# Optimization experiments

Measured on AMD Instinct MI355X. Metric: run time of the kernel, lower is better.

Reference implementation:

```python
import jax, jax.numpy as jnp
import numpy as np

C = 128
N0, N1, N2 = 1000000, 100000, 10000


def setup_inputs() -> dict:
    key = jax.random.key(0)
    ks = jax.random.split(key, 9)
    return {
        "x0": jax.random.normal(ks[0], (N0, C), dtype=jnp.float32),
        "x1": jax.random.normal(ks[1], (N1, C), dtype=jnp.float32),
        "x2": jax.random.normal(ks[2], (N2, C), dtype=jnp.float32),
        "cluster1": jax.random.randint(ks[3], (N0,), 0, N1, dtype=jnp.int32),
        "cluster2": jax.random.randint(ks[4], (N1,), 0, N2, dtype=jnp.int32),
        "Wf2c0": jax.random.normal(ks[5], (C, C), dtype=jnp.float32) / np.sqrt(C),
        "Wf2c1": jax.random.normal(ks[6], (C, C), dtype=jnp.float32) / np.sqrt(C),
        "Wc2f0": jax.random.normal(ks[7], (C, C), dtype=jnp.float32) / np.sqrt(C),
        "Wc2f1": jax.random.normal(ks[8], (C, C), dtype=jnp.float32) / np.sqrt(C),
    }


def _segment_mean(x, idx, num_segments):
    # scatter-mean: sum per cluster / count (count clamped to 1 -> empty clusters give 0)
    s = jax.ops.segment_sum(x, idx, num_segments=num_segments)
    cnt = jax.ops.segment_sum(jnp.ones((x.shape[0], 1), x.dtype), idx, num_segments=num_segments)
    return s / jnp.maximum(cnt, 1.0)


def reference(x0, x1, x2, cluster1, cluster2, Wf2c0, Wf2c1, Wc2f0, Wc2f1):
    n1, n2 = x1.shape[0], x2.shape[0]
    # scale 0: x0 + gather(coarse_to_fine_0(x1), cluster1)
    y0 = x0 + (x1 @ Wc2f0.T)[cluster1]
    # scale 1: x1 + fine_to_coarse_0(scatter_mean(x0, cluster1)) + gather(coarse_to_fine_1(x2), cluster2)
    y1 = x1 + _segment_mean(x0, cluster1, n1) @ Wf2c0.T + (x2 @ Wc2f1.T)[cluster2]
    # scale 2: x2 + fine_to_coarse_1(scatter_mean(x1, cluster2))
    y2 = x2 + _segment_mean(x1, cluster2, n2) @ Wf2c1.T
    return (y0, y1, y2)
```

## Files before the change

kernel.cpp:

```cpp
#include <hip/hip_runtime.h>

#define C128 128

typedef __attribute__((ext_vector_type(2))) float f32x2;
typedef __attribute__((ext_vector_type(4))) float f32x4;
typedef __attribute__((ext_vector_type(8))) short short8;

__device__ __forceinline__ short f2bf(float f) {
  union { float f; unsigned u; } v; v.f = f;
  unsigned r = (v.u + 0x7fffu + ((v.u >> 16) & 1u)) >> 16;
  return (short)r;
}

__global__ __launch_bounds__(256) void prep(
    const float* __restrict__ Wa, const float* __restrict__ Wb_,
    const float* __restrict__ Wc, const float* __restrict__ Wd,
    ushort* __restrict__ Wout, int* __restrict__ zbuf, int zlen)
{
  const int tid = blockIdx.x * 256 + threadIdx.x;
  const int nth = gridDim.x * 256;
  for (int k = tid; k < zlen; k += nth) zbuf[k] = 0;
  for (int k = tid; k < 4 * 16384; k += nth) {
    const float* W = (k < 16384) ? Wa : (k < 32768) ? Wb_ : (k < 49152) ? Wc : Wd;
    Wout[k] = (ushort)f2bf(W[k & 16383]);
  }
}

__device__ __forceinline__ void gemm_body(
    const float* __restrict__ A, const ushort* __restrict__ Wb,
    const float* __restrict__ add,
    const int* __restrict__ gidx, const float* __restrict__ gtab,
    float* __restrict__ out, int R, int blockrow)
{
  const int tid  = threadIdx.x;
  const int wave = tid >> 6;
  const int lane = tid & 63;
  const int r16  = lane & 15;
  const int kg   = lane >> 4;

  const int rowbase = blockrow + wave * 16;
  if (rowbase >= R) return;
  const int arow_i  = rowbase + r16;
  const int lrow    = arow_i < R ? arow_i : (R - 1);

  f32x4 acc[8];
#pragma unroll
  for (int i = 0; i < 8; ++i) acc[i] = (f32x4){0.f, 0.f, 0.f, 0.f};

  const float* arow = A + (long long)lrow * C128;

#pragma unroll
  for (int ks = 0; ks < 4; ++ks) {
    const int k0 = ks * 32 + kg * 8;
    f32x4 alo = *(const f32x4*)(arow + k0);
    f32x4 ahi = *(const f32x4*)(arow + k0 + 4);
    short8 af;
    af[0] = f2bf(alo.x); af[1] = f2bf(alo.y);
    af[2] = f2bf(alo.z); af[3] = f2bf(alo.w);
    af[4] = f2bf(ahi.x); af[5] = f2bf(ahi.y);
    af[6] = f2bf(ahi.z); af[7] = f2bf(ahi.w);
#pragma unroll
    for (int nf = 0; nf < 8; ++nf) {
      short8 bf = *(const short8*)(Wb + (nf * 16 + r16) * C128 + k0);
      acc[nf] = __builtin_amdgcn_mfma_f32_16x16x32_bf16(af, bf, acc[nf], 0, 0, 0);
    }
  }

#pragma unroll
  for (int i = 0; i < 4; ++i) {
    const int orow = rowbase + kg * 4 + i;
    if (orow >= R) continue;
    const float* addrow = add ? add + (long long)orow * C128 : nullptr;
    const float* grow = gidx ? gtab + (long long)gidx[orow] * C128 : nullptr;
    float* orow_p = out + (long long)orow * C128;
#pragma unroll
    for (int nf = 0; nf < 8; ++nf) {
      const int oc = nf * 16 + r16;
      float v = acc[nf][i];
      if (addrow) v += addrow[oc];
      if (grow)   v += grow[oc];
      orow_p[oc] = v;
    }
  }
}

__global__ __launch_bounds__(256) void pre_hist_gemm(
    const float* __restrict__ x1, const ushort* __restrict__ W1b, float* __restrict__ t1, int n1,
    const float* __restrict__ x2, const ushort* __restrict__ W2b, float* __restrict__ t2, int n2,
    const int* __restrict__ cl1, int n0, int* __restrict__ cnt0,
    const int* __restrict__ cl2, int* __restrict__ cnt1, int B1)
{
  {
    int i = blockIdx.x * 256 + threadIdx.x;
    const int nth = gridDim.x * 256;
    const int total = n0 + n1;
    for (; i < total; i += nth) {
      if (i < n0) atomicAdd(&cnt0[cl1[i]], 1);
      else        atomicAdd(&cnt1[cl2[i - n0]], 1);
    }
  }
  if ((int)blockIdx.x < B1)
    gemm_body(x1, W1b, nullptr, nullptr, nullptr, t1, n1, blockIdx.x * 64);
  else
    gemm_body(x2, W2b, nullptr, nullptr, nullptr, t2, n2, (blockIdx.x - B1) * 64);
}

__global__ __launch_bounds__(256) void post_gemm(
    const float* __restrict__ mean0, const ushort* __restrict__ Wab,
    const float* __restrict__ x1, const int* __restrict__ cluster2,
    const float* __restrict__ t2, float* __restrict__ y1, int n1,
    const float* __restrict__ mean1, const ushort* __restrict__ Wbb,
    const float* __restrict__ x2, float* __restrict__ y2, int n2, int B1)
{
  if ((int)blockIdx.x < B1)
    gemm_body(mean0, Wab, x1, cluster2, t2, y1, n1, blockIdx.x * 64);
  else
    gemm_body(mean1, Wbb, x2, nullptr, nullptr, y2, n2, (blockIdx.x - B1) * 64);
}

__global__ __launch_bounds__(256) void scan2(
    const int* __restrict__ cnt0, int* __restrict__ off0, int* __restrict__ cur0, int n1,
    const int* __restrict__ cnt1, int* __restrict__ off1, int* __restrict__ cur1, int n2,
    int* __restrict__ tot)
{
  const int p1 = (n1 + 255) & ~255;
  const int i  = blockIdx.x * blockDim.x + threadIdx.x;
  const int lane = threadIdx.x & 63;

  const int* cnt; int* off; int* cur; int* t; int j; int nn;
  if (i < p1) { cnt = cnt0; off = off0; cur = cur0; t = tot + 0; j = i;      nn = n1; }
  else        { cnt = cnt1; off = off1; cur = cur1; t = tot + 1; j = i - p1; nn = n2; }

  int c = (j < nn) ? cnt[j] : 0;
  int pref = c;
#pragma unroll
  for (int d = 1; d < 64; d <<= 1) {
    int v = __shfl_up(pref, d);
    if (lane >= d) pref += v;
  }
  const int wave_total = __shfl(pref, 63);
  int base = 0;
  if (lane == 63) base = atomicAdd(t, wave_total);
  base = __shfl(base, 63);

  if (j < nn) {
    const int o = base + (pref - c);
    off[j] = o;
    cur[j] = o;
  }
}

__global__ __launch_bounds__(256) void fill2(
    const int* __restrict__ cl1, int n0, int* __restrict__ cur0, int* __restrict__ idx0,
    const int* __restrict__ cl2, int n1, int* __restrict__ cur1, int* __restrict__ idx1)
{
  int i = blockIdx.x * blockDim.x + threadIdx.x;
  const int stride = gridDim.x * blockDim.x;
  const int total = n0 + n1;
  for (; i < total; i += stride) {
    if (i < n0) { int p = atomicAdd(&cur0[cl1[i]], 1); idx0[p] = i; }
    else        { int k = i - n0; int p = atomicAdd(&cur1[cl2[k]], 1); idx1[p] = k; }
  }
}

__device__ __forceinline__ void cr_one(
    int wid, int lane, const float* __restrict__ x,
    const int* __restrict__ idxp, const int* __restrict__ offp,
    const int* __restrict__ cntp, const float* __restrict__ trow,
    float* __restrict__ yb, float* __restrict__ meanp)
{
  const int n = cntp[wid];
  const int o = offp[wid];

  f32x2 tc = {0.f, 0.f};
  if (trow) tc = ((const f32x2*)trow)[lane];

  f32x2 s0 = {0.f,0.f}, s1 = {0.f,0.f}, s2 = {0.f,0.f}, s3 = {0.f,0.f};
  for (int base = 0; base < n; base += 64) {
    int m = n - base; if (m > 64) m = 64;
    int vi = (lane < m) ? idxp[o + base + lane] : 0;
    int j = 0;
    for (; j + 3 < m; j += 4) {
      const long long i0 = __shfl(vi, j);
      const long long i1 = __shfl(vi, j + 1);
      const long long i2 = __shfl(vi, j + 2);
      const long long i3 = __shfl(vi, j + 3);
      f32x2 a = ((const f32x2*)(x + i0 * C128))[lane];
      f32x2 b = ((const f32x2*)(x + i1 * C128))[lane];
      f32x2 c = ((const f32x2*)(x + i2 * C128))[lane];
      f32x2 d = ((const f32x2*)(x + i3 * C128))[lane];
      s0 += a; s1 += b; s2 += c; s3 += d;
      if (yb) {
        ((f32x2*)(yb + i0 * C128))[lane] = a + tc;
        ((f32x2*)(yb + i1 * C128))[lane] = b + tc;
        ((f32x2*)(yb + i2 * C128))[lane] = c + tc;
        ((f32x2*)(yb + i3 * C128))[lane] = d + tc;
      }
    }
    for (; j < m; ++j) {
      const long long i0 = __shfl(vi, j);
      f32x2 a = ((const f32x2*)(x + i0 * C128))[lane];
      s0 += a;
      if (yb) ((f32x2*)(yb + i0 * C128))[lane] = a + tc;
    }
  }

  const float invn = n > 0 ? 1.0f / (float)n : 0.0f;
  ((f32x2*)(meanp + (long long)wid * C128))[lane] = ((s0 + s1) + (s2 + s3)) * invn;
}

__global__ __launch_bounds__(256) void cluster_reduce2(
    const float* __restrict__ x0, const int* __restrict__ idx0,
    const int* __restrict__ off0, const int* __restrict__ cnt0,
    const float* __restrict__ t1, float* __restrict__ y0,
    float* __restrict__ mean0, int n1,
    const float* __restrict__ x1, const int* __restrict__ idx1,
    const int* __restrict__ off1, const int* __restrict__ cnt1,
    float* __restrict__ mean1, int n2)
{
  const int wid  = blockIdx.x * 4 + (threadIdx.x >> 6);
  const int lane = threadIdx.x & 63;
  if (wid >= n1 + n2) return;

  if (wid < n1)
    cr_one(wid, lane, x0, idx0, off0, cnt0,
           t1 + (long long)wid * C128, y0, mean0);
  else
    cr_one(wid - n1, lane, x1, idx1, off1, cnt1,
           nullptr, nullptr, mean1);
}

extern "C" void kernel_launch(void* const* d_in, const int* in_sizes, int n_in,
                              void* d_out, int out_size, void* d_ws, size_t ws_size,
                              hipStream_t stream)
{
  const float* x0 = (const float*)d_in[0];
  const float* x1 = (const float*)d_in[1];
  const float* x2 = (const float*)d_in[2];
  const int* cluster1 = (const int*)d_in[3];
  const int* cluster2 = (const int*)d_in[4];
  const float* Wf2c0 = (const float*)d_in[5];
  const float* Wf2c1 = (const float*)d_in[6];
  const float* Wc2f0 = (const float*)d_in[7];
  const float* Wc2f1 = (const float*)d_in[8];

  const int N0 = in_sizes[0] / C128;
  const int N1 = in_sizes[1] / C128;
  const int N2 = in_sizes[2] / C128;

  float* y0 = (float*)d_out;
  float* y1 = y0 + (long long)N0 * C128;
  float* y2 = y1 + (long long)N1 * C128;

  float* mean0 = y1;
  float* mean1 = y2;

  float* t1 = (float*)d_ws;
  float* t2 = t1 + (long long)N1 * C128;
  int* cnt0 = (int*)(t2 + (long long)N2 * C128);
  int* cnt1 = cnt0 + N1;
  int* tot  = cnt1 + N2;
  int* off0 = tot + 2;
  int* off1 = off0 + N1;
  int* cur0 = off1 + N2;
  int* cur1 = cur0 + N1;
  int* idx0 = cur1 + N2;
  int* idx1 = idx0 + N0;
  ushort* Wb = (ushort*)(idx1 + N1);
  ushort* Wb_c2f0 = Wb;
  ushort* Wb_c2f1 = Wb + 16384;
  ushort* Wb_f2c0 = Wb + 32768;
  ushort* Wb_f2c1 = Wb + 49152;

  const int B1 = (N1 + 63) / 64;
  const int B2 = (N2 + 63) / 64;

  prep<<<256, 256, 0, stream>>>(
      Wc2f0, Wc2f1, Wf2c0, Wf2c1, Wb, cnt0, N1 + N2 + 2);

  pre_hist_gemm<<<B1 + B2, 256, 0, stream>>>(
      x1, Wb_c2f0, t1, N1, x2, Wb_c2f1, t2, N2,
      cluster1, N0, cnt0, cluster2, cnt1, B1);

  const int p1 = (N1 + 255) & ~255, p2 = (N2 + 255) & ~255;
  scan2<<<(p1 + p2) / 256, 256, 0, stream>>>(
      cnt0, off0, cur0, N1, cnt1, off1, cur1, N2, tot);
  int bh = (N0 + N1 + 255) / 256; if (bh > 2048) bh = 2048;
  fill2<<<bh, 256, 0, stream>>>(cluster1, N0, cur0, idx0, cluster2, N1, cur1, idx1);

  cluster_reduce2<<<(N1 + N2 + 3) / 4, 256, 0, stream>>>(
      x0, idx0, off0, cnt0, t1, y0, mean0, N1,
      x1, idx1, off1, cnt1, mean1, N2);

  post_gemm<<<B1 + B2, 256, 0, stream>>>(
      mean0, Wb_f2c0, x1, cluster2, t2, y1, N1,
      mean1, Wb_f2c1, x2, y2, N2, B1);
}
```

Measured before the change: 499.3 us.

## Stream x0 sequentially into bf16 cluster bins instead of gathering by index

Replaces the fill-index plus gathered cluster reduce with a streaming pass. It reads x0/x1 rows in order, writes y0, and scatters bf16 copies of each row into per-cluster bins using atomic cursors. A second kernel then reduces the contiguous bins into bf16 means, which feed the post GEMM directly as bf16 A operands. The goal is to swap random full-precision gathers of x0 for sequential reads and half-size scattered writes. The cost is extra workspace, a bf16 rounding of the inputs before summation, and a fallback path when the workspace is too small.

```diff
diff --git a/kernel.cpp b/kernel.cpp
--- a/kernel.cpp
+++ b/kernel.cpp
@@ -10,6 +10,12 @@
   union { float f; unsigned u; } v; v.f = f;
   unsigned r = (v.u + 0x7fffu + ((v.u >> 16) & 1u)) >> 16;
   return (short)r;
+}
+
+__device__ __forceinline__ f32x2 bfp2f(unsigned u) {
+  union { unsigned u; float f; } a, b;
+  a.u = u << 16; b.u = u & 0xffff0000u;
+  return (f32x2){a.f, b.f};
 }
 
 __global__ __launch_bounds__(256) void prep(
@@ -26,8 +32,9 @@
   }
 }
 
+template <typename AT>
 __device__ __forceinline__ void gemm_body(
-    const float* __restrict__ A, const ushort* __restrict__ Wb,
+    const AT* __restrict__ A, const ushort* __restrict__ Wb,
     const float* __restrict__ add,
     const int* __restrict__ gidx, const float* __restrict__ gtab,
     float* __restrict__ out, int R, int blockrow)
@@ -47,18 +54,22 @@
 #pragma unroll
   for (int i = 0; i < 8; ++i) acc[i] = (f32x4){0.f, 0.f, 0.f, 0.f};
 
-  const float* arow = A + (long long)lrow * C128;
+  const AT* arow = A + (long long)lrow * C128;
 
 #pragma unroll
   for (int ks = 0; ks < 4; ++ks) {
     const int k0 = ks * 32 + kg * 8;
-    f32x4 alo = *(const f32x4*)(arow + k0);
-    f32x4 ahi = *(const f32x4*)(arow + k0 + 4);
     short8 af;
-    af[0] = f2bf(alo.x); af[1] = f2bf(alo.y);
-    af[2] = f2bf(alo.z); af[3] = f2bf(alo.w);
-    af[4] = f2bf(ahi.x); af[5] = f2bf(ahi.y);
-    af[6] = f2bf(ahi.z); af[7] = f2bf(ahi.w);
+    if constexpr (sizeof(AT) == 2) {
+      af = *(const short8*)((const ushort*)arow + k0);
+    } else {
+      f32x4 alo = *(const f32x4*)((const float*)arow + k0);
+      f32x4 ahi = *(const f32x4*)((const float*)arow + k0 + 4);
+      af[0] = f2bf(alo.x); af[1] = f2bf(alo.y);
+      af[2] = f2bf(alo.z); af[3] = f2bf(alo.w);
+      af[4] = f2bf(ahi.x); af[5] = f2bf(ahi.y);
+      af[6] = f2bf(ahi.z); af[7] = f2bf(ahi.w);
+    }
 #pragma unroll
     for (int nf = 0; nf < 8; ++nf) {
       short8 bf = *(const short8*)(Wb + (nf * 16 + r16) * C128 + k0);
@@ -100,22 +111,9 @@
     }
   }
   if ((int)blockIdx.x < B1)
-    gemm_body(x1, W1b, nullptr, nullptr, nullptr, t1, n1, blockIdx.x * 64);
+    gemm_body<float>(x1, W1b, nullptr, nullptr, nullptr, t1, n1, blockIdx.x * 64);
   else
-    gemm_body(x2, W2b, nullptr, nullptr, nullptr, t2, n2, (blockIdx.x - B1) * 64);
-}
-
-__global__ __launch_bounds__(256) void post_gemm(
-    const float* __restrict__ mean0, const ushort* __restrict__ Wab,
-    const float* __restrict__ x1, const int* __restrict__ cluster2,
-    const float* __restrict__ t2, float* __restrict__ y1, int n1,
-    const float* __restrict__ mean1, const ushort* __restrict__ Wbb,
-    const float* __restrict__ x2, float* __restrict__ y2, int n2, int B1)
-{
-  if ((int)blockIdx.x < B1)
-    gemm_body(mean0, Wab, x1, cluster2, t2, y1, n1, blockIdx.x * 64);
-  else
-    gemm_body(mean1, Wbb, x2, nullptr, nullptr, y2, n2, (blockIdx.x - B1) * 64);
+    gemm_body<float>(x2, W2b, nullptr, nullptr, nullptr, t2, n2, (blockIdx.x - B1) * 64);
 }
 
 __global__ __launch_bounds__(256) void scan2(
@@ -149,6 +147,92 @@
     cur[j] = o;
   }
 }
+
+
+__global__ __launch_bounds__(256) void stream_bin(
+    const float* __restrict__ x0, const int* __restrict__ cl1,
+    const float* __restrict__ t1, float* __restrict__ y0,
+    int* __restrict__ cur0, ushort* __restrict__ bin0, int n0,
+    const float* __restrict__ x1, const int* __restrict__ cl2,
+    int* __restrict__ cur1, ushort* __restrict__ bin1, int n1)
+{
+  const int wid0 = blockIdx.x * 4 + (threadIdx.x >> 6);
+  const int nw   = gridDim.x * 4;
+  const int lane = threadIdx.x & 63;
+  const int total = n0 + n1;
+  for (int r = wid0; r < total; r += nw) {
+    if (r < n0) {
+      const int c = cl1[r];
+      int pos = 0;
+      if (lane == 0) pos = atomicAdd(&cur0[c], 1);
+      pos = __shfl(pos, 0);
+      f32x2 xv = ((const f32x2*)(x0 + (long long)r * C128))[lane];
+      f32x2 tv = ((const f32x2*)(t1 + (long long)c * C128))[lane];
+      ((f32x2*)(y0 + (long long)r * C128))[lane] = xv + tv;
+      unsigned p = ((unsigned)(ushort)f2bf(xv.x)) | (((unsigned)(ushort)f2bf(xv.y)) << 16);
+      ((unsigned*)bin0)[(long long)pos * 64 + lane] = p;
+    } else {
+      const int rr = r - n0;
+      const int c = cl2[rr];
+      int pos = 0;
+      if (lane == 0) pos = atomicAdd(&cur1[c], 1);
+      pos = __shfl(pos, 0);
+      f32x2 xv = ((const f32x2*)(x1 + (long long)rr * C128))[lane];
+      unsigned p = ((unsigned)(ushort)f2bf(xv.x)) | (((unsigned)(ushort)f2bf(xv.y)) << 16);
+      ((unsigned*)bin1)[(long long)pos * 64 + lane] = p;
+    }
+  }
+}
+
+__global__ __launch_bounds__(256) void reduce_bins(
+    const ushort* __restrict__ bin0, const int* __restrict__ off0,
+    const int* __restrict__ cnt0, ushort* __restrict__ mb0, int n1,
+    const ushort* __restrict__ bin1, const int* __restrict__ off1,
+    const int* __restrict__ cnt1, ushort* __restrict__ mb1, int n2)
+{
+  int wid = blockIdx.x * 4 + (threadIdx.x >> 6);
+  const int lane = threadIdx.x & 63;
+  if (wid >= n1 + n2) return;
+
+  const ushort* bin; const int* off; const int* cnt; ushort* mb;
+  if (wid < n1) { bin = bin0; off = off0; cnt = cnt0; mb = mb0; }
+  else { wid -= n1; bin = bin1; off = off1; cnt = cnt1; mb = mb1; }
+
+  const int n = cnt[wid];
+  const long long o = off[wid];
+
+  f32x2 s0 = {0.f,0.f}, s1 = {0.f,0.f}, s2 = {0.f,0.f}, s3 = {0.f,0.f};
+  int m = 0;
+  for (; m + 3 < n; m += 4) {
+    unsigned a = ((const unsigned*)bin)[(o + m) * 64 + lane];
+    unsigned b = ((const unsigned*)bin)[(o + m + 1) * 64 + lane];
+    unsigned c = ((const unsigned*)bin)[(o + m + 2) * 64 + lane];
+    unsigned d = ((const unsigned*)bin)[(o + m + 3) * 64 + lane];
+    s0 += bfp2f(a); s1 += bfp2f(b); s2 += bfp2f(c); s3 += bfp2f(d);
+  }
+  for (; m < n; ++m)
+    s0 += bfp2f(((const unsigned*)bin)[(o + m) * 64 + lane]);
+
+  f32x2 s = (s0 + s1) + (s2 + s3);
+  const float invn = n > 0 ? 1.0f / (float)n : 0.0f;
+  s *= invn;
+  unsigned p = ((unsigned)(ushort)f2bf(s.x)) | (((unsigned)(ushort)f2bf(s.y)) << 16);
+  ((unsigned*)mb)[(long long)wid * 64 + lane] = p;
+}
+
+__global__ __launch_bounds__(256) void post_gemm_b(
+    const ushort* __restrict__ mb0, const ushort* __restrict__ Wab,
+    const float* __restrict__ x1, const int* __restrict__ cluster2,
+    const float* __restrict__ t2, float* __restrict__ y1, int n1,
+    const ushort* __restrict__ mb1, const ushort* __restrict__ Wbb,
+    const float* __restrict__ x2, float* __restrict__ y2, int n2, int B1)
+{
+  if ((int)blockIdx.x < B1)
+    gemm_body<ushort>(mb0, Wab, x1, cluster2, t2, y1, n1, blockIdx.x * 64);
+  else
+    gemm_body<ushort>(mb1, Wbb, x2, nullptr, nullptr, y2, n2, (blockIdx.x - B1) * 64);
+}
+
 
 __global__ __launch_bounds__(256) void fill2(
     const int* __restrict__ cl1, int n0, int* __restrict__ cur0, int* __restrict__ idx0,
@@ -230,6 +314,19 @@
            nullptr, nullptr, mean1);
 }
 
+__global__ __launch_bounds__(256) void post_gemm_f(
+    const float* __restrict__ mean0, const ushort* __restrict__ Wab,
+    const float* __restrict__ x1, const int* __restrict__ cluster2,
+    const float* __restrict__ t2, float* __restrict__ y1, int n1,
+    const float* __restrict__ mean1, const ushort* __restrict__ Wbb,
+    const float* __restrict__ x2, float* __restrict__ y2, int n2, int B1)
+{
+  if ((int)blockIdx.x < B1)
+    gemm_body<float>(mean0, Wab, x1, cluster2, t2, y1, n1, blockIdx.x * 64);
+  else
+    gemm_body<float>(mean1, Wbb, x2, nullptr, nullptr, y2, n2, (blockIdx.x - B1) * 64);
+}
+
 extern "C" void kernel_launch(void* const* d_in, const int* in_sizes, int n_in,
                               void* d_out, int out_size, void* d_ws, size_t ws_size,
                               hipStream_t stream)
@@ -252,31 +349,44 @@
   float* y1 = y0 + (long long)N0 * C128;
   float* y2 = y1 + (long long)N1 * C128;
 
-  float* mean0 = y1;
-  float* mean1 = y2;
-
-  float* t1 = (float*)d_ws;
-  float* t2 = t1 + (long long)N1 * C128;
-  int* cnt0 = (int*)(t2 + (long long)N2 * C128);
-  int* cnt1 = cnt0 + N1;
-  int* tot  = cnt1 + N2;
-  int* off0 = tot + 2;
-  int* off1 = off0 + N1;
-  int* cur0 = off1 + N2;
-  int* cur1 = cur0 + N1;
-  int* idx0 = cur1 + N2;
-  int* idx1 = idx0 + N0;
-  ushort* Wb = (ushort*)(idx1 + N1);
-  ushort* Wb_c2f0 = Wb;
-  ushort* Wb_c2f1 = Wb + 16384;
-  ushort* Wb_f2c0 = Wb + 32768;
-  ushort* Wb_f2c1 = Wb + 49152;
+  float* wsf = (float*)d_ws;
+  long long o = 0;
+  float* t1 = wsf + o;          o += (long long)N1 * C128;
+  float* t2 = wsf + o;          o += (long long)N2 * C128;
+  int* cnt0 = (int*)(wsf + o);  o += N1;
+  int* cnt1 = (int*)(wsf + o);  o += N2;
+  int* tot  = (int*)(wsf + o);  o += 2;
+  int* off0 = (int*)(wsf + o);  o += N1;
+  int* off1 = (int*)(wsf + o);  o += N2;
+  int* cur0 = (int*)(wsf + o);  o += N1;
+  int* cur1 = (int*)(wsf + o);  o += N2;
+  const long long head = o;
+
+  long long oa = (head + 7) & ~7LL;
+  ushort* Wb  = (ushort*)(wsf + oa); oa += 4 * 16384 / 2;
+  ushort* mb0 = (ushort*)(wsf + oa); oa += (long long)N1 * 64;
+  ushort* mb1 = (ushort*)(wsf + oa); oa += (long long)N2 * 64;
+  ushort* bin0 = (ushort*)(wsf + oa); oa += (long long)N0 * 64;
+  ushort* bin1 = (ushort*)(wsf + oa); oa += (long long)N1 * 64;
+  const size_t needA = (size_t)oa * 4;
+
+  long long ob = head;
+  int* idx0 = (int*)(wsf + ob); ob += N0;
+  int* idx1 = (int*)(wsf + ob); ob += N1;
+  ob = (ob + 7) & ~7LL;
+  ushort* WbB = (ushort*)(wsf + ob); ob += 4 * 16384 / 2;
 
   const int B1 = (N1 + 63) / 64;
   const int B2 = (N2 + 63) / 64;
+  const bool bigws = ws_size >= needA;
+  ushort* Wp = bigws ? Wb : WbB;
+  ushort* Wb_c2f0 = Wp;
+  ushort* Wb_c2f1 = Wp + 16384;
+  ushort* Wb_f2c0 = Wp + 32768;
+  ushort* Wb_f2c1 = Wp + 49152;
 
   prep<<<256, 256, 0, stream>>>(
-      Wc2f0, Wc2f1, Wf2c0, Wf2c1, Wb, cnt0, N1 + N2 + 2);
+      Wc2f0, Wc2f1, Wf2c0, Wf2c1, Wp, cnt0, N1 + N2 + 2);
 
   pre_hist_gemm<<<B1 + B2, 256, 0, stream>>>(
       x1, Wb_c2f0, t1, N1, x2, Wb_c2f1, t2, N2,
@@ -285,14 +395,27 @@
   const int p1 = (N1 + 255) & ~255, p2 = (N2 + 255) & ~255;
   scan2<<<(p1 + p2) / 256, 256, 0, stream>>>(
       cnt0, off0, cur0, N1, cnt1, off1, cur1, N2, tot);
-  int bh = (N0 + N1 + 255) / 256; if (bh > 2048) bh = 2048;
-  fill2<<<bh, 256, 0, stream>>>(cluster1, N0, cur0, idx0, cluster2, N1, cur1, idx1);
-
-  cluster_reduce2<<<(N1 + N2 + 3) / 4, 256, 0, stream>>>(
-      x0, idx0, off0, cnt0, t1, y0, mean0, N1,
-      x1, idx1, off1, cnt1, mean1, N2);
-
-  post_gemm<<<B1 + B2, 256, 0, stream>>>(
-      mean0, Wb_f2c0, x1, cluster2, t2, y1, N1,
-      mean1, Wb_f2c1, x2, y2, N2, B1);
-}
+
+  if (bigws) {
+    stream_bin<<<2048, 256, 0, stream>>>(
+        x0, cluster1, t1, y0, cur0, bin0, N0,
+        x1, cluster2, cur1, bin1, N1);
+    reduce_bins<<<(N1 + N2 + 3) / 4, 256, 0, stream>>>(
+        bin0, off0, cnt0, mb0, N1,
+        bin1, off1, cnt1, mb1, N2);
+    post_gemm_b<<<B1 + B2, 256, 0, stream>>>(
+        mb0, Wb_f2c0, x1, cluster2, t2, y1, N1,
+        mb1, Wb_f2c1, x2, y2, N2, B1);
+  } else {
+    float* mean0 = y1;
+    float* mean1 = y2;
+    int bh = (N0 + N1 + 255) / 256; if (bh > 2048) bh = 2048;
+    fill2<<<bh, 256, 0, stream>>>(cluster1, N0, cur0, idx0, cluster2, N1, cur1, idx1);
+    cluster_reduce2<<<(N1 + N2 + 3) / 4, 256, 0, stream>>>(
+        x0, idx0, off0, cnt0, t1, y0, mean0, N1,
+        x1, idx1, off1, cnt1, mean1, N2);
+    post_gemm_f<<<B1 + B2, 256, 0, stream>>>(
+        mean0, Wb_f2c0, x1, cluster2, t2, y1, N1,
+        mean1, Wb_f2c1, x2, y2, N2, B1);
+  }
+}
```

New measurement: 677.2 us. 1.36x slower.

## Regroup launches: fuse histogram with weight conversion, fill with pre-GEMM

Applied to the files above, without the earlier changes.

Moves the cluster histogram into the weight-conversion kernel (zeroing is now a memset) and merges the index-fill pass into the pre-GEMM kernel, so the fill's atomics overlap with the x1/x2 projection GEMMs instead of running as a separate launch. This removes one kernel launch and one serialized pass. It also adds an 8-way unrolled gather loop in the cluster reduce to keep more loads in flight, and aligns the bf16 weight buffer in the workspace. The fill now runs on B1+B2 blocks rather than a capped grid, and the extra unroll raises register pressure.

```diff
diff --git a/kernel.cpp b/kernel.cpp
--- a/kernel.cpp
+++ b/kernel.cpp
@@ -12,17 +12,55 @@
   return (short)r;
 }
 
-__global__ __launch_bounds__(256) void prep(
+__global__ __launch_bounds__(256) void hist_wconv(
+    const int* __restrict__ cl1, int n0, int* __restrict__ cnt0,
+    const int* __restrict__ cl2, int n1, int* __restrict__ cnt1,
     const float* __restrict__ Wa, const float* __restrict__ Wb_,
     const float* __restrict__ Wc, const float* __restrict__ Wd,
-    ushort* __restrict__ Wout, int* __restrict__ zbuf, int zlen)
+    ushort* __restrict__ Wout)
 {
   const int tid = blockIdx.x * 256 + threadIdx.x;
   const int nth = gridDim.x * 256;
-  for (int k = tid; k < zlen; k += nth) zbuf[k] = 0;
   for (int k = tid; k < 4 * 16384; k += nth) {
     const float* W = (k < 16384) ? Wa : (k < 32768) ? Wb_ : (k < 49152) ? Wc : Wd;
     Wout[k] = (ushort)f2bf(W[k & 16383]);
+  }
+  const int total = n0 + n1;
+  for (int i = tid; i < total; i += nth) {
+    if (i < n0) atomicAdd(&cnt0[cl1[i]], 1);
+    else        atomicAdd(&cnt1[cl2[i - n0]], 1);
+  }
+}
+
+__global__ __launch_bounds__(256) void scan2(
+    const int* __restrict__ cnt0, int* __restrict__ off0, int* __restrict__ cur0, int n1,
+    const int* __restrict__ cnt1, int* __restrict__ off1, int* __restrict__ cur1, int n2,
+    int* __restrict__ tot)
+{
+  const int p1 = (n1 + 255) & ~255;
+  const int i  = blockIdx.x * blockDim.x + threadIdx.x;
+  const int lane = threadIdx.x & 63;
+
+  const int* cnt; int* off; int* cur; int* t; int j; int nn;
+  if (i < p1) { cnt = cnt0; off = off0; cur = cur0; t = tot + 0; j = i;      nn = n1; }
+  else        { cnt = cnt1; off = off1; cur = cur1; t = tot + 1; j = i - p1; nn = n2; }
+
+  int c = (j < nn) ? cnt[j] : 0;
+  int pref = c;
+#pragma unroll
+  for (int d = 1; d < 64; d <<= 1) {
+    int v = __shfl_up(pref, d);
+    if (lane >= d) pref += v;
+  }
+  const int wave_total = __shfl(pref, 63);
+  int base = 0;
+  if (lane == 63) base = atomicAdd(t, wave_total);
+  base = __shfl(base, 63);
+
+  if (j < nn) {
+    const int o = base + (pref - c);
+    off[j] = o;
+    cur[j] = o;
   }
 }
 
@@ -84,83 +122,26 @@
   }
 }
 
-__global__ __launch_bounds__(256) void pre_hist_gemm(
-    const float* __restrict__ x1, const ushort* __restrict__ W1b, float* __restrict__ t1, int n1,
-    const float* __restrict__ x2, const ushort* __restrict__ W2b, float* __restrict__ t2, int n2,
-    const int* __restrict__ cl1, int n0, int* __restrict__ cnt0,
-    const int* __restrict__ cl2, int* __restrict__ cnt1, int B1)
+__global__ __launch_bounds__(256) void fill_pregemm(
+    const int* __restrict__ cl1, int n0, int* __restrict__ cur0, int* __restrict__ idx0,
+    const int* __restrict__ cl2, int n1, int* __restrict__ cur1, int* __restrict__ idx1,
+    const float* __restrict__ x1, const ushort* __restrict__ W1b, float* __restrict__ t1,
+    const float* __restrict__ x2, const ushort* __restrict__ W2b, float* __restrict__ t2,
+    int n2, int B1)
 {
   {
     int i = blockIdx.x * 256 + threadIdx.x;
     const int nth = gridDim.x * 256;
     const int total = n0 + n1;
     for (; i < total; i += nth) {
-      if (i < n0) atomicAdd(&cnt0[cl1[i]], 1);
-      else        atomicAdd(&cnt1[cl2[i - n0]], 1);
+      if (i < n0) { int p = atomicAdd(&cur0[cl1[i]], 1); idx0[p] = i; }
+      else        { int k = i - n0; int p = atomicAdd(&cur1[cl2[k]], 1); idx1[p] = k; }
     }
   }
   if ((int)blockIdx.x < B1)
     gemm_body(x1, W1b, nullptr, nullptr, nullptr, t1, n1, blockIdx.x * 64);
   else
     gemm_body(x2, W2b, nullptr, nullptr, nullptr, t2, n2, (blockIdx.x - B1) * 64);
-}
-
-__global__ __launch_bounds__(256) void post_gemm(
-    const float* __restrict__ mean0, const ushort* __restrict__ Wab,
-    const float* __restrict__ x1, const int* __restrict__ cluster2,
-    const float* __restrict__ t2, float* __restrict__ y1, int n1,
-    const float* __restrict__ mean1, const ushort* __restrict__ Wbb,
-    const float* __restrict__ x2, float* __restrict__ y2, int n2, int B1)
-{
-  if ((int)blockIdx.x < B1)
-    gemm_body(mean0, Wab, x1, cluster2, t2, y1, n1, blockIdx.x * 64);
-  else
-    gemm_body(mean1, Wbb, x2, nullptr, nullptr, y2, n2, (blockIdx.x - B1) * 64);
-}
-
-__global__ __launch_bounds__(256) void scan2(
-    const int* __restrict__ cnt0, int* __restrict__ off0, int* __restrict__ cur0, int n1,
-    const int* __restrict__ cnt1, int* __restrict__ off1, int* __restrict__ cur1, int n2,
-    int* __restrict__ tot)
-{
-  const int p1 = (n1 + 255) & ~255;
-  const int i  = blockIdx.x * blockDim.x + threadIdx.x;
-  const int lane = threadIdx.x & 63;
-
-  const int* cnt; int* off; int* cur; int* t; int j; int nn;
-  if (i < p1) { cnt = cnt0; off = off0; cur = cur0; t = tot + 0; j = i;      nn = n1; }
-  else        { cnt = cnt1; off = off1; cur = cur1; t = tot + 1; j = i - p1; nn = n2; }
-
-  int c = (j < nn) ? cnt[j] : 0;
-  int pref = c;
-#pragma unroll
-  for (int d = 1; d < 64; d <<= 1) {
-    int v = __shfl_up(pref, d);
-    if (lane >= d) pref += v;
-  }
-  const int wave_total = __shfl(pref, 63);
-  int base = 0;
-  if (lane == 63) base = atomicAdd(t, wave_total);
-  base = __shfl(base, 63);
-
-  if (j < nn) {
-    const int o = base + (pref - c);
-    off[j] = o;
-    cur[j] = o;
-  }
-}
-
-__global__ __launch_bounds__(256) void fill2(
-    const int* __restrict__ cl1, int n0, int* __restrict__ cur0, int* __restrict__ idx0,
-    const int* __restrict__ cl2, int n1, int* __restrict__ cur1, int* __restrict__ idx1)
-{
-  int i = blockIdx.x * blockDim.x + threadIdx.x;
-  const int stride = gridDim.x * blockDim.x;
-  const int total = n0 + n1;
-  for (; i < total; i += stride) {
-    if (i < n0) { int p = atomicAdd(&cur0[cl1[i]], 1); idx0[p] = i; }
-    else        { int k = i - n0; int p = atomicAdd(&cur1[cl2[k]], 1); idx1[p] = k; }
-  }
 }
 
 __device__ __forceinline__ void cr_one(
@@ -180,6 +161,36 @@
     int m = n - base; if (m > 64) m = 64;
     int vi = (lane < m) ? idxp[o + base + lane] : 0;
     int j = 0;
+    for (; j + 7 < m; j += 8) {
+      const long long i0 = __shfl(vi, j);
+      const long long i1 = __shfl(vi, j + 1);
+      const long long i2 = __shfl(vi, j + 2);
+      const long long i3 = __shfl(vi, j + 3);
+      const long long i4 = __shfl(vi, j + 4);
+      const long long i5 = __shfl(vi, j + 5);
+      const long long i6 = __shfl(vi, j + 6);
+      const long long i7 = __shfl(vi, j + 7);
+      f32x2 a = ((const f32x2*)(x + i0 * C128))[lane];
+      f32x2 b = ((const f32x2*)(x + i1 * C128))[lane];
+      f32x2 c = ((const f32x2*)(x + i2 * C128))[lane];
+      f32x2 d = ((const f32x2*)(x + i3 * C128))[lane];
+      f32x2 e = ((const f32x2*)(x + i4 * C128))[lane];
+      f32x2 f = ((const f32x2*)(x + i5 * C128))[lane];
+      f32x2 g = ((const f32x2*)(x + i6 * C128))[lane];
+      f32x2 h = ((const f32x2*)(x + i7 * C128))[lane];
+      s0 += a; s1 += b; s2 += c; s3 += d;
+      s0 += e; s1 += f; s2 += g; s3 += h;
+      if (yb) {
+        ((f32x2*)(yb + i0 * C128))[lane] = a + tc;
+        ((f32x2*)(yb + i1 * C128))[lane] = b + tc;
+        ((f32x2*)(yb + i2 * C128))[lane] = c + tc;
+        ((f32x2*)(yb + i3 * C128))[lane] = d + tc;
+        ((f32x2*)(yb + i4 * C128))[lane] = e + tc;
+        ((f32x2*)(yb + i5 * C128))[lane] = f + tc;
+        ((f32x2*)(yb + i6 * C128))[lane] = g + tc;
+        ((f32x2*)(yb + i7 * C128))[lane] = h + tc;
+      }
+    }
     for (; j + 3 < m; j += 4) {
       const long long i0 = __shfl(vi, j);
       const long long i1 = __shfl(vi, j + 1);
@@ -230,6 +241,19 @@
            nullptr, nullptr, mean1);
 }
 
+__global__ __launch_bounds__(256) void post_gemm(
+    const float* __restrict__ mean0, const ushort* __restrict__ Wab,
+    const float* __restrict__ x1, const int* __restrict__ cluster2,
+    const float* __restrict__ t2, float* __restrict__ y1, int n1,
+    const float* __restrict__ mean1, const ushort* __restrict__ Wbb,
+    const float* __restrict__ x2, float* __restrict__ y2, int n2, int B1)
+{
+  if ((int)blockIdx.x < B1)
+    gemm_body(mean0, Wab, x1, cluster2, t2, y1, n1, blockIdx.x * 64);
+  else
+    gemm_body(mean1, Wbb, x2, nullptr, nullptr, y2, n2, (blockIdx.x - B1) * 64);
+}
+
 extern "C" void kernel_launch(void* const* d_in, const int* in_sizes, int n_in,
                               void* d_out, int out_size, void* d_ws, size_t ws_size,
                               hipStream_t stream)
@@ -255,18 +279,21 @@
   float* mean0 = y1;
   float* mean1 = y2;
 
-  float* t1 = (float*)d_ws;
-  float* t2 = t1 + (long long)N1 * C128;
-  int* cnt0 = (int*)(t2 + (long long)N2 * C128);
-  int* cnt1 = cnt0 + N1;
-  int* tot  = cnt1 + N2;
-  int* off0 = tot + 2;
-  int* off1 = off0 + N1;
-  int* cur0 = off1 + N2;
-  int* cur1 = cur0 + N1;
-  int* idx0 = cur1 + N2;
-  int* idx1 = idx0 + N0;
-  ushort* Wb = (ushort*)(idx1 + N1);
+  float* wsf = (float*)d_ws;
+  long long o = 0;
+  float* t1 = wsf + o;          o += (long long)N1 * C128;
+  float* t2 = wsf + o;          o += (long long)N2 * C128;
+  int* cnt0 = (int*)(wsf + o);  o += N1;
+  int* cnt1 = (int*)(wsf + o);  o += N2;
+  int* tot  = (int*)(wsf + o);  o += 2;
+  int* off0 = (int*)(wsf + o);  o += N1;
+  int* off1 = (int*)(wsf + o);  o += N2;
+  int* cur0 = (int*)(wsf + o);  o += N1;
+  int* cur1 = (int*)(wsf + o);  o += N2;
+  int* idx0 = (int*)(wsf + o);  o += N0;
+  int* idx1 = (int*)(wsf + o);  o += N1;
+  o = (o + 7) & ~7LL;
+  ushort* Wb = (ushort*)(wsf + o);
   ushort* Wb_c2f0 = Wb;
   ushort* Wb_c2f1 = Wb + 16384;
   ushort* Wb_f2c0 = Wb + 32768;
@@ -275,18 +302,19 @@
   const int B1 = (N1 + 63) / 64;
   const int B2 = (N2 + 63) / 64;
 
-  prep<<<256, 256, 0, stream>>>(
-      Wc2f0, Wc2f1, Wf2c0, Wf2c1, Wb, cnt0, N1 + N2 + 2);
-
-  pre_hist_gemm<<<B1 + B2, 256, 0, stream>>>(
-      x1, Wb_c2f0, t1, N1, x2, Wb_c2f1, t2, N2,
-      cluster1, N0, cnt0, cluster2, cnt1, B1);
+  hipMemsetAsync(cnt0, 0, (size_t)(N1 + N2 + 2) * 4, stream);
+  int bh = (N0 + N1 + 255) / 256; if (bh > 1024) bh = 1024;
+  hist_wconv<<<bh, 256, 0, stream>>>(
+      cluster1, N0, cnt0, cluster2, N1, cnt1,
+      Wc2f0, Wc2f1, Wf2c0, Wf2c1, Wb);
 
   const int p1 = (N1 + 255) & ~255, p2 = (N2 + 255) & ~255;
   scan2<<<(p1 + p2) / 256, 256, 0, stream>>>(
       cnt0, off0, cur0, N1, cnt1, off1, cur1, N2, tot);
-  int bh = (N0 + N1 + 255) / 256; if (bh > 2048) bh = 2048;
-  fill2<<<bh, 256, 0, stream>>>(cluster1, N0, cur0, idx0, cluster2, N1, cur1, idx1);
+
+  fill_pregemm<<<B1 + B2, 256, 0, stream>>>(
+      cluster1, N0, cur0, idx0, cluster2, N1, cur1, idx1,
+      x1, Wb_c2f0, t1, x2, Wb_c2f1, t2, N2, B1);
 
   cluster_reduce2<<<(N1 + N2 + 3) / 4, 256, 0, stream>>>(
       x0, idx0, off0, cnt0, t1, y0, mean0, N1,
```

After: 485.0 us. -2.9%, faster.
